# Kernel tuning notes

Measured on AMD Instinct MI355X. Metric: run time of the kernel, lower is better.

## Reference

```python
import jax, jax.numpy as jnp
import numpy as np

B, C, H, W = 16, 256, 56, 56
HID = C * 2            # modifier_expansion = 2
GROUPS = 8             # min(8, HID//4)
K = 3                  # inner_steps
LR = 0.01              # exp(log(inner_lr))
RATIO = 0.25           # spatial_mask_ratio
GN_EPS = 1e-5


def setup_inputs() -> dict:
    key = jax.random.key(0)
    ks = jax.random.split(key, 12)
    x = jax.random.normal(ks[0], (B, C, H, W), jnp.float32)
    # modifier params (1x1 convs stored as 2D matrices) + GroupNorm affine
    conv1_w = jax.random.normal(ks[1], (HID, C), jnp.float32) / np.sqrt(C)
    gn_gamma = 1.0 + 0.1 * jax.random.normal(ks[2], (HID,), jnp.float32)
    gn_beta = 0.1 * jax.random.normal(ks[3], (HID,), jnp.float32)
    conv2_w = jax.random.normal(ks[4], (C, HID), jnp.float32) / np.sqrt(HID)
    # surprise reconstructor (bottleneck = C//4)
    recon_w1 = jax.random.normal(ks[5], (C // 4, C), jnp.float32) / np.sqrt(C)
    recon_w2 = jax.random.normal(ks[6], (C, C // 4), jnp.float32) / np.sqrt(C // 4)
    # gate MLP
    gate_w1 = jax.random.normal(ks[7], (C // 4, C), jnp.float32) / np.sqrt(C)
    gate_b1 = jnp.zeros((C // 4,), jnp.float32)
    gate_w2 = jax.random.normal(ks[8], (1, C // 4), jnp.float32) / np.sqrt(C // 4)
    gate_b2 = jnp.zeros((1,), jnp.float32)
    residual_scale = jnp.asarray(0.05, jnp.float32)
    # EMA buffers (eval mode: frozen)
    running_mean = 0.05 * jax.random.normal(ks[9], (C,), jnp.float32)
    running_var = 1.0 + 0.05 * jax.random.uniform(ks[10], (C,), jnp.float32)
    # spatial masks: exactly int(H*W*RATIO) zeroed positions per sample, one mask
    # per inner update step (only steps 0..K-2 affect the output)
    num_mask = int(H * W * RATIO)
    rng = np.random.default_rng(0)
    r = rng.random((K - 1, B, H * W))
    idx = np.argsort(r, axis=-1)[..., :num_mask]
    m = np.ones((K - 1, B, H * W), dtype=bool)
    np.put_along_axis(m, idx, False, axis=-1)
    masks = jnp.asarray(m.reshape(K - 1, B, 1, H, W))
    return dict(x=x, conv1_w=conv1_w, gn_gamma=gn_gamma, gn_beta=gn_beta,
                conv2_w=conv2_w, recon_w1=recon_w1, recon_w2=recon_w2,
                gate_w1=gate_w1, gate_b1=gate_b1, gate_w2=gate_w2,
                gate_b2=gate_b2, residual_scale=residual_scale,
                running_mean=running_mean, running_var=running_var, masks=masks)


def _group_norm(h, gamma, beta):
    b = h.shape[0]
    hg = h.reshape(b, GROUPS, HID // GROUPS, H, W)
    mu = hg.mean(axis=(2, 3, 4), keepdims=True)
    var = hg.var(axis=(2, 3, 4), keepdims=True)  # biased, matching torch GN
    hg = (hg - mu) * jax.lax.rsqrt(var + GN_EPS)
    return hg.reshape(b, HID, H, W) * gamma[None, :, None, None] + beta[None, :, None, None]


def _modifier(feat, w1, gamma, beta, w2):
    # Conv2d 1x1 (no bias) -> GroupNorm -> GELU -> [Dropout2d: identity in eval] -> Conv2d 1x1
    h = jnp.einsum('bchw,oc->bohw', feat, w1)
    h = jax.nn.gelu(_group_norm(h, gamma, beta), approximate=False)
    return jnp.einsum('bohw,co->bchw', h, w2)


def _surprise(y, mask, rw1, rw2, rm, rv):
    mf = mask.astype(y.dtype)                       # [B,1,H,W]
    my = y * mf
    h = jax.nn.gelu(jnp.einsum('bchw,oc->bohw', my, rw1), approximate=False)
    rec = jnp.einsum('bohw,co->bchw', h, rw2)
    inv = 1.0 - mf
    recon = (((rec - y) ** 2) * inv).sum() / (inv.sum() * C + 1e-8)
    n = y.shape[0] * y.shape[2] * y.shape[3]
    cm = y.mean(axis=(0, 2, 3))                     # [C]
    cv = ((y - cm[None, :, None, None]) ** 2).sum(axis=(0, 2, 3)) / (n - 1)  # unbiased
    consist = ((cm - rm) ** 2).mean() + ((cv / (rv + 1e-8) - 1.0) ** 2).mean()
    return recon + 0.1 * consist


def reference(x, conv1_w, gn_gamma, gn_beta, conv2_w, recon_w1, recon_w2,
              gate_w1, gate_b1, gate_w2, gate_b2, residual_scale,
              running_mean, running_var, masks):
    feat = jax.lax.stop_gradient(x)  # feat_inner = features.detach()
    params = (conv1_w, gn_gamma, gn_beta, conv2_w)

    def inner_loss(p, mask):
        m = _modifier(feat, *p)
        return _surprise(m + feat, mask, recon_w1, recon_w2, running_mean, running_var)

    # TTT inner loop: K-1 SGD updates on the modifier params; updates are
    # stop_gradient'ed so the outer Jacobian wrt initial params is identity,
    # matching torch's .data in-place update with create_graph=False.
    for step in range(K - 1):
        g = jax.grad(inner_loss)(params, masks[step])
        params = tuple(p - LR * jax.lax.stop_gradient(gi) for p, gi in zip(params, g))

    modification = _modifier(x, *params)  # final forward uses non-detached features

    pooled = x.mean(axis=(2, 3))                                    # [B,C]
    gh = jax.nn.gelu(pooled @ gate_w1.T + gate_b1, approximate=False)
    gate = jax.nn.sigmoid(gh @ gate_w2.T + gate_b2)[:, :, None, None]  # [B,1,1,1]

    return x + residual_scale * gate * modification
```

## Files before the change

### kernel.cpp

```cpp
#include <hip/hip_runtime.h>
#include <math.h>


#define BB    16
#define CC    256
#define HWW   3136
#define NTOT  (BB*HWW)
#define HIDD  512
#define NGRP  8
#define GMSZ  (64*HWW)
#define C4    64
#define LRATE 0.01f
#define SKW   32
#define CHUNK (NTOT/SKW)
#define NV8   (HWW/8)
#define FSTR  132

#define EP_STORE    0
#define EP_ADDFEAT  1
#define EP_T1H      2
#define EP_DYREC    3
#define EP_DT1      4
#define EP_DYFIN    5
#define EP_H1STAT   6
#define EP_YADDSTAT 7
#define EP_GNB1     8
#define EP_OUT      9

typedef unsigned short u16;
typedef __attribute__((ext_vector_type(8))) short bf16x8;
typedef __attribute__((ext_vector_type(4))) float f32x4;

__device__ __forceinline__ float bf2f(u16 u){
  return __uint_as_float(((unsigned)u)<<16);
}
__device__ __forceinline__ u16 f2bf(float f){
  unsigned u = __float_as_uint(f);
  u += 0x7FFFu + ((u>>16)&1u);
  return (u16)(u>>16);
}
__device__ __forceinline__ float gelu_f(float x){
  return 0.5f*x*(1.0f+erff(x*0.70710678118654752f));
}
__device__ __forceinline__ float rcp_f(float x){ return __builtin_amdgcn_rcpf(x); }
__device__ __forceinline__ float gelu_fast(float x){
  float x2 = x*x;
  float u = 0.7978845608f*x*fmaf(0.044715f, x2, 1.0f);
  float t = 1.0f - 2.0f*rcp_f(__expf(2.0f*u)+1.0f);
  return 0.5f*x*(1.0f+t);
}
__device__ __forceinline__ float gelu_g_fast(float x){
  float x2 = x*x;
  float u = 0.7978845608f*x*fmaf(0.044715f, x2, 1.0f);
  float t = 1.0f - 2.0f*rcp_f(__expf(2.0f*u)+1.0f);
  float du = 0.7978845608f*fmaf(0.134145f, x2, 1.0f);
  return fmaf(0.5f*x*(1.0f-t*t), du, 0.5f*(1.0f+t));
}
__device__ __forceinline__ float blk_sum(float v, float* sm){
  #pragma unroll
  for (int o=32;o>0;o>>=1) v += __shfl_down(v,o);
  if ((threadIdx.x & 63)==0) sm[threadIdx.x>>6] = v;
  __syncthreads();
  float r = sm[0]+sm[1]+sm[2]+sm[3];
  __syncthreads();
  return r;
}
__device__ __forceinline__ uint4 pack8(const ushort* e){
  uint4 v;
  v.x = (unsigned)e[0] | ((unsigned)e[1]<<16);
  v.y = (unsigned)e[2] | ((unsigned)e[3]<<16);
  v.z = (unsigned)e[4] | ((unsigned)e[5]<<16);
  v.w = (unsigned)e[6] | ((unsigned)e[7]<<16);
  return v;
}
__device__ __forceinline__ void up8(uint4 v, float* f){
  f[0]=bf2f((u16)(v.x&0xFFFFu)); f[1]=bf2f((u16)(v.x>>16));
  f[2]=bf2f((u16)(v.y&0xFFFFu)); f[3]=bf2f((u16)(v.y>>16));
  f[4]=bf2f((u16)(v.z&0xFFFFu)); f[5]=bf2f((u16)(v.z>>16));
  f[6]=bf2f((u16)(v.w&0xFFFFu)); f[7]=bf2f((u16)(v.w>>16));
}
__device__ __forceinline__ uint4 pk8(const float* f){
  uint4 v;
  v.x=(unsigned)f2bf(f[0])|((unsigned)f2bf(f[1])<<16);
  v.y=(unsigned)f2bf(f[2])|((unsigned)f2bf(f[3])<<16);
  v.z=(unsigned)f2bf(f[4])|((unsigned)f2bf(f[5])<<16);
  v.w=(unsigned)f2bf(f[6])|((unsigned)f2bf(f[7])<<16);
  return v;
}

__global__ void k_detect_dtype(const u16* __restrict__ xs, int* flag){
  if (threadIdx.x || blockIdx.x) return;
  int plaus = 0;
  for (int i=0;i<256;i+=2){
    float f = bf2f(xs[i]);
    float a = fabsf(f);
    if (isfinite(f) && a < 32.0f && a > 1e-5f) plaus++;
  }
  *flag = (plaus >= 64) ? 1 : 0;
}
__global__ void k_detect_mask(const unsigned char* __restrict__ m, int* flag){
  if (threadIdx.x || blockIdx.x) return;
  unsigned char mx=0; int nz0=0,nz1=0,nz2=0,nz3=0;
  for (int i=0;i<256;i++){
    unsigned char v=m[i]; if (v>mx) mx=v;
    if (v){ int r=i&3; if(r==0)nz0=1; else if(r==1)nz1=1; else if(r==2)nz2=1; else nz3=1; }
  }
  int f;
  if (mx<=1) f = (nz1|nz2|nz3) ? 0 : 1;
  else       f = (!nz0 && !nz1) ? 3 : 2;
  *flag=f;
}
__global__ void k_report(u16* out, float v){
  if (threadIdx.x==0 && blockIdx.x==0) out[0] = f2bf(v);
}

__global__ void k_cvt(const void* __restrict__ src, float* __restrict__ dst, int n,
                      const int* __restrict__ dtf){
  int i = blockIdx.x*256 + threadIdx.x;
  if (i>=n) return;
  if (*dtf) dst[i] = bf2f(((const u16*)src)[i]);
  else      dst[i] = ((const float*)src)[i];
}
__global__ void k_wcvt(const float* __restrict__ src, u16* __restrict__ d,
                       u16* __restrict__ dT, int R, int Cc){
  int i = blockIdx.x*256+threadIdx.x;
  if (i >= R*Cc) return;
  int r = i/Cc, c = i - r*Cc;
  u16 v = f2bf(src[i]);
  d[i] = v;
  if (dT) dT[(size_t)c*R + r] = v;
}

__global__ void k_expand(const unsigned char* __restrict__ mraw, const int* __restrict__ flag,
                         float* __restrict__ mf, float* __restrict__ zc){
  __shared__ float sm[4];
  int i = blockIdx.x*256 + threadIdx.x;
  int f = *flag;
  float v;
  if (f==1)      v = (((const int*)mraw)[i] != 0) ? 1.f : 0.f;
  else if (f==0) v = (mraw[i] != 0) ? 1.f : 0.f;
  else if (f==2) v = (((const u16*)mraw)[i] != 0) ? 1.f : 0.f;
  else           v = (((const float*)mraw)[i] != 0.f) ? 1.f : 0.f;
  mf[i] = v;
  float S = blk_sum(1.f - v, sm);
  if (threadIdx.x==0) atomicAdd(&zc[blockIdx.x/196], S);
}

template<int MASKX,int EPI,int XDYN,int E0DYN,int MT,int XGN>
__global__ __launch_bounds__(256) void k_gemm_mfma(
    const u16* __restrict__ A, const void* __restrict__ Xv, u16* __restrict__ Out,
    int K, const int* __restrict__ xdt, const float* __restrict__ mf,
    const void* __restrict__ e0, const float* __restrict__ e1,
    const float* __restrict__ e2, u16* __restrict__ o2, float* __restrict__ o3,
    const float* __restrict__ xmu, const float* __restrict__ xpg)
{
  constexpr int MROWS = 64*MT;
  constexpr int NMI   = 4*MT;
  __shared__ __align__(16) u16 Ws[MROWS*42];
  __shared__ __align__(16) u16 Xs[128*42];
  const int t = threadIdx.x;
  const int w = t >> 6, lane = t & 63;
  const int col = lane & 15, quad = lane >> 4;
  const int M = (int)gridDim.y * MROWS;
  const int m0 = blockIdx.y * MROWS, n0 = blockIdx.x << 7;
  const int isbx = XDYN ? *xdt : 1;
  const u16*   Xb = (const u16*)Xv;
  const float* Xf = (const float*)Xv;
  const int wrow = t >> 2, wkq = (t & 3) * 8;
  const int xn   = 2*(t & 63);
  const int xq   = t >> 6;
  const int gn0  = n0 + xn;
  const int xb_  = gn0 / HWW;
  const int xs_  = gn0 - xb_*HWW;

  f32x4 acc[NMI][2];
  #pragma unroll
  for (int i=0;i<NMI;i++){
    #pragma unroll
    for (int j=0;j<2;j++) acc[i][j] = (f32x4)(0.0f);
  }

  for (int k0=0; k0<K; k0+=32){
    if (MT==2){
      const u16* ap = A + (size_t)(m0 + (t>>1))*K + k0 + (t&1)*16;
      *(uint4*)(Ws + (t>>1)*42 + (t&1)*16)     = *(const uint4*)ap;
      *(uint4*)(Ws + (t>>1)*42 + (t&1)*16 + 8) = *(const uint4*)(ap+8);
    } else {
      uint4 v = *(const uint4*)(A + (size_t)(m0+wrow)*K + k0 + wkq);
      *(uint4*)(Ws + wrow*42 + wkq) = v;
    }
    {
      ushort e[16];
      size_t base = ((size_t)xb_*K + k0 + xq*8)*HWW + xs_;
      if (isbx){
        #pragma unroll
        for (int j=0;j<8;j++){
          unsigned v = *(const unsigned*)(Xb + base + (size_t)j*HWW);
          if (XGN){
            const int o  = k0 + xq*8 + j;
            const int bg = xb_*NGRP + (o>>6);
            const float mu_ = xmu[bg], rs_ = xmu[128+bg];
            const float ga_ = xpg[o],  be_ = xpg[512+o];
            float f0 = bf2f((u16)(v & 0xFFFFu));
            float f1 = bf2f((u16)(v >> 16));
            f0 = fmaf((f0-mu_)*rs_, ga_, be_);
            f1 = fmaf((f1-mu_)*rs_, ga_, be_);
            f0 = (XGN==2) ? gelu_f(f0) : gelu_fast(f0);
            f1 = (XGN==2) ? gelu_f(f1) : gelu_fast(f1);
            e[j]   = f2bf(f0);
            e[8+j] = f2bf(f1);
          } else {
            e[j]   = (ushort)(v & 0xFFFFu);
            e[8+j] = (ushort)(v >> 16);
          }
        }
      } else {
        #pragma unroll
        for (int j=0;j<8;j++){
          float2 f = *(const float2*)(Xf + base + (size_t)j*HWW);
          e[j]   = f2bf(f.x);
          e[8+j] = f2bf(f.y);
        }
      }
      if (MASKX){
        if (mf[gn0]   == 0.f){
          #pragma unroll
          for (int j=0;j<8;j++) e[j] = 0;
        }
        if (mf[gn0+1] == 0.f){
          #pragma unroll
          for (int j=0;j<8;j++) e[8+j] = 0;
        }
      }
      *(uint4*)(Xs + xn*42     + xq*8) = pack8(e);
      *(uint4*)(Xs + (xn+1)*42 + xq*8) = pack8(e+8);
    }
    __syncthreads();
    bf16x8 bfr[2];
    #pragma unroll
    for (int nj=0;nj<2;nj++)
      bfr[nj] = *(const bf16x8*)(Xs + (w*32+nj*16+col)*42 + quad*8);
    #pragma unroll
    for (int mi=0;mi<NMI;mi++){
      bf16x8 af = *(const bf16x8*)(Ws + (mi*16+col)*42 + quad*8);
      acc[mi][0] = __builtin_amdgcn_mfma_f32_16x16x32_bf16(af, bfr[0], acc[mi][0], 0,0,0);
      acc[mi][1] = __builtin_amdgcn_mfma_f32_16x16x32_bf16(af, bfr[1], acc[mi][1], 0,0,0);
    }
    __syncthreads();
  }
  const int isb0 = E0DYN ? *xdt : 1;
  float* fst  = (float*)Xs;
  float* sred = (float*)Ws;
  const int row16 = t >> 4;
  const int cb    = (t & 15) * 8;
  const int nb8   = n0 + cb;
  const int b8    = nb8 / HWW;
  const int sb8   = nb8 - b8*HWW;
  const int bA    = n0 / HWW, bB = (n0+127)/HWW;
  const int gbase = m0 >> 6;

  if (EPI==EP_H1STAT){ if (t < 4*MT) sred[t]=0.f; }
  if (EPI==EP_GNB1){ if (t < 4*MT) sred[2*NMI*16 + t]=0.f; }
  if (EPI==EP_H1STAT||EPI==EP_GNB1) __syncthreads();

  float dscale=0.f, gmul=0.f;
  if (EPI==EP_DYREC) dscale = 2.0f / (e1[0]*(float)CC + 1e-8f);
  if (EPI==EP_OUT)   gmul = e2[0]*e1[b8];
  float hs0[MT], hq0[MT], hs1[MT], hq1[MT];
  #pragma unroll
  for (int i=0;i<MT;i++){ hs0[i]=0.f; hq0[i]=0.f; hs1[i]=0.f; hq1[i]=0.f; }

  #pragma unroll
  for (int mi=0;mi<NMI;mi++){
    #pragma unroll
    for (int nj=0;nj<2;nj++){
      #pragma unroll
      for (int r=0;r<4;r++)
        fst[(quad*4+r)*FSTR + w*32 + nj*16 + col] = acc[mi][nj][r];
    }
    __syncthreads();
    const int m = m0 + mi*16 + row16;
    const size_t oidx = ((size_t)b8*M + m)*HWW + sb8;
    float v[8];
    {
      const float* frow = fst + row16*FSTR + cb;
      float4 p0 = *(const float4*)frow;
      float4 p1 = *(const float4*)(frow+4);
      v[0]=p0.x; v[1]=p0.y; v[2]=p0.z; v[3]=p0.w;
      v[4]=p1.x; v[5]=p1.y; v[6]=p1.z; v[7]=p1.w;
    }

    if (EPI==EP_STORE){
      *(uint4*)(Out+oidx) = pk8(v);
    }
    else if (EPI==EP_ADDFEAT){
      float xv[8];
      if (isb0) up8(*(const uint4*)((const u16*)e0+oidx), xv);
      else {
        float4 a0 = *(const float4*)((const float*)e0+oidx);
        float4 a1 = *(const float4*)((const float*)e0+oidx+4);
        xv[0]=a0.x; xv[1]=a0.y; xv[2]=a0.z; xv[3]=a0.w;
        xv[4]=a1.x; xv[5]=a1.y; xv[6]=a1.z; xv[7]=a1.w;
      }
      #pragma unroll
      for (int j=0;j<8;j++) v[j] += xv[j];
      *(uint4*)(Out+oidx) = pk8(v);
    }
    else if (EPI==EP_T1H){
      *(uint4*)(Out+oidx) = pk8(v);
      float gv[8];
      #pragma unroll
      for (int j=0;j<8;j++) gv[j] = gelu_fast(v[j]);
      *(uint4*)(o2+oidx) = pk8(gv);
    }
    else if (EPI==EP_DYREC){
      float yv[8], mfv[8];
      up8(*(const uint4*)((const u16*)e0+oidx), yv);
      float4 f0 = *(const float4*)(mf+nb8);
      float4 f1 = *(const float4*)(mf+nb8+4);
      mfv[0]=f0.x; mfv[1]=f0.y; mfv[2]=f0.z; mfv[3]=f0.w;
      mfv[4]=f1.x; mfv[5]=f1.y; mfv[6]=f1.z; mfv[7]=f1.w;
      #pragma unroll
      for (int j=0;j<8;j++) v[j] = (v[j]-yv[j])*(1.0f-mfv[j])*dscale;
      *(uint4*)(Out+oidx) = pk8(v);
    }
    else if (EPI==EP_DT1){
      float tv[8];
      up8(*(const uint4*)((const u16*)e0+oidx), tv);
      #pragma unroll
      for (int j=0;j<8;j++) v[j] = v[j]*gelu_g_fast(tv[j]);
      *(uint4*)(Out+oidx) = pk8(v);
    }
    else if (EPI==EP_DYFIN){
      float yv[8], dv[8], mfv[8];
      up8(*(const uint4*)((const u16*)e0+oidx), yv);
      up8(*(const uint4*)(Out+oidx), dv);
      float4 f0 = *(const float4*)(mf+nb8);
      float4 f1 = *(const float4*)(mf+nb8+4);
      mfv[0]=f0.x; mfv[1]=f0.y; mfv[2]=f0.z; mfv[3]=f0.w;
      mfv[4]=f1.x; mfv[5]=f1.y; mfv[6]=f1.z; mfv[7]=f1.w;
      const float c1 = e1[m], c2 = e2[m];
      #pragma unroll
      for (int j=0;j<8;j++) v[j] = mfv[j]*v[j] - dv[j] + c1 + c2*yv[j];
      *(uint4*)(Out+oidx) = pk8(v);
    }
    else if (EPI==EP_H1STAT){
      *(uint4*)(Out+oidx) = pk8(v);
      float s=0.f, q=0.f;
      #pragma unroll
      for (int j=0;j<8;j++){ s += v[j]; q = fmaf(v[j],v[j],q); }
      const bool inA = (b8==bA);
      hs0[mi>>2] += inA ? s : 0.f;  hq0[mi>>2] += inA ? q : 0.f;
      hs1[mi>>2] += inA ? 0.f : s;  hq1[mi>>2] += inA ? 0.f : q;
    }
    else if (EPI==EP_YADDSTAT){
      float xv[8];
      if (isb0) up8(*(const uint4*)((const u16*)e0+oidx), xv);
      else {
        float4 a0 = *(const float4*)((const float*)e0+oidx);
        float4 a1 = *(const float4*)((const float*)e0+oidx+4);
        xv[0]=a0.x; xv[1]=a0.y; xv[2]=a0.z; xv[3]=a0.w;
        xv[4]=a1.x; xv[5]=a1.y; xv[6]=a1.z; xv[7]=a1.w;
      }
      float s=0.f, q=0.f;
      #pragma unroll
      for (int j=0;j<8;j++){
        v[j] += xv[j];
        s += v[j]; q = fmaf(v[j],v[j],q);
      }
      *(uint4*)(Out+oidx) = pk8(v);
      #pragma unroll
      for (int o=1;o<16;o<<=1){ s += __shfl_xor(s,o); q += __shfl_xor(q,o); }
      if ((t&15)==0){
        sred[mi*16+row16]          = s;
        sred[NMI*16 + mi*16+row16] = q;
      }
    }
    else if (EPI==EP_GNB1){
      float hv[8];
      up8(*(const uint4*)((const u16*)e0+oidx), hv);
      const int gcur = gbase + (mi>>2);
      const float muT = e1[b8*NGRP+gcur], rT = e1[128+b8*NGRP+gcur];
      const float go = e2[m], beo = e2[HIDD+m];
      float dB=0.f, dG=0.f, sS=0.f, sQ=0.f;
      #pragma unroll
      for (int j=0;j<8;j++){
        float hn   = (hv[j]-muT)*rT;
        float ghat = fmaf(hn, go, beo);
        float dgh  = v[j]*gelu_g_fast(ghat);
        float dhn  = dgh*go;
        v[j] = dhn;
        dB += dgh; dG = fmaf(dgh,hn,dG);
        sS += dhn; sQ = fmaf(dhn,hn,sQ);
      }
      *(uint4*)(Out+oidx) = pk8(v);
      #pragma unroll
      for (int o=1;o<16;o<<=1){ dB += __shfl_xor(dB,o); dG += __shfl_xor(dG,o); }
      if ((t&15)==0){
        sred[mi*16+row16]          = dB;
        sred[NMI*16 + mi*16+row16] = dG;
      }
      const bool inA = (b8==bA);
      hs0[mi>>2] += inA ? sS : 0.f;  hq0[mi>>2] += inA ? sQ : 0.f;
      hs1[mi>>2] += inA ? 0.f : sS;  hq1[mi>>2] += inA ? 0.f : sQ;
    }
    else if (EPI==EP_OUT){
      float xv[8];
      if (isb0){
        up8(*(const uint4*)((const u16*)e0+oidx), xv);
        #pragma unroll
        for (int j=0;j<8;j++) v[j] = xv[j] + gmul*v[j];
        *(uint4*)(Out+oidx) = pk8(v);
      } else {
        float4 a0 = *(const float4*)((const float*)e0+oidx);
        float4 a1 = *(const float4*)((const float*)e0+oidx+4);
        float4 r0, r1;
        r0.x = a0.x + gmul*v[0]; r0.y = a0.y + gmul*v[1];
        r0.z = a0.z + gmul*v[2]; r0.w = a0.w + gmul*v[3];
        r1.x = a1.x + gmul*v[4]; r1.y = a1.y + gmul*v[5];
        r1.z = a1.z + gmul*v[6]; r1.w = a1.w + gmul*v[7];
        *(float4*)((float*)Out+oidx)   = r0;
        *(float4*)((float*)Out+oidx+4) = r1;
      }
    }
    __syncthreads();
  }

  if (EPI==EP_H1STAT || EPI==EP_GNB1){
    const int soff = (EPI==EP_GNB1) ? 2*NMI*16 : 0;
    #pragma unroll
    for (int g2=0; g2<MT; g2++){
      float a0=hs0[g2], c0=hq0[g2], a1=hs1[g2], c1=hq1[g2];
      #pragma unroll
      for (int o=1;o<64;o<<=1){
        a0 += __shfl_xor(a0,o); c0 += __shfl_xor(c0,o);
        a1 += __shfl_xor(a1,o); c1 += __shfl_xor(c1,o);
      }
      if (lane==0){
        atomicAdd(&sred[soff+g2*4+0], a0);
        atomicAdd(&sred[soff+g2*4+1], c0);
        atomicAdd(&sred[soff+g2*4+2], a1);
        atomicAdd(&sred[soff+g2*4+3], c1);
      }
    }
    __syncthreads();
  }

  if (EPI==EP_H1STAT){
    if (t==0){
      #pragma unroll
      for (int g2=0; g2<MT; g2++){
        atomicAdd(&o3[bA*NGRP+gbase+g2],     sred[g2*4+0]);
        atomicAdd(&o3[128+bA*NGRP+gbase+g2], sred[g2*4+1]);
      }
    }
    if (t==1 && bB!=bA){
      #pragma unroll
      for (int g2=0; g2<MT; g2++){
        atomicAdd(&o3[bB*NGRP+gbase+g2],     sred[g2*4+2]);
        atomicAdd(&o3[128+bB*NGRP+gbase+g2], sred[g2*4+3]);
      }
    }
  }
  if (EPI==EP_YADDSTAT){
    if (t < NMI*16){
      atomicAdd(&o3[m0+t],    sred[t]);
      atomicAdd(&o3[CC+m0+t], sred[NMI*16+t]);
    }
  }
  if (EPI==EP_GNB1){
    if (t < NMI*16){
      atomicAdd(&o3[m0+t],     sred[NMI*16+t]);
      atomicAdd(&o3[512+m0+t], sred[t]);
    }
    if (t==NMI*16){
      #pragma unroll
      for (int g2=0; g2<MT; g2++){
        atomicAdd(&o3[1024+bA*NGRP+gbase+g2], sred[2*NMI*16+g2*4+0]);
        atomicAdd(&o3[1152+bA*NGRP+gbase+g2], sred[2*NMI*16+g2*4+1]);
      }
    }
    if (t==NMI*16+1 && bB!=bA){
      #pragma unroll
      for (int g2=0; g2<MT; g2++){
        atomicAdd(&o3[1024+bB*NGRP+gbase+g2], sred[2*NMI*16+g2*4+2]);
        atomicAdd(&o3[1152+bB*NGRP+gbase+g2], sred[2*NMI*16+g2*4+3]);
      }
    }
  }
}

template<int QDYN, int GNB2>
__global__ __launch_bounds__(256) void k_wgrad_mfma(
    const u16* __restrict__ P, const void* __restrict__ Qv, float* __restrict__ part,
    int CHP, int CHQ, const int* __restrict__ xdt, int ntx,
    const u16* __restrict__ h1, const float* __restrict__ musig,
    const float* __restrict__ red)
{
  __shared__ __align__(16) u16 Ps[64*42];
  __shared__ __align__(16) u16 Qs[64*42];
  const int f = blockIdx.x;
  const int j = f >> 3;
  const int sk = (f & 7) + ((j >> 5) << 3);
  const int tile = j & 31;
  const int ty = tile / ntx;
  const int m0 = (tile - ty*ntx) << 6;
  const int n0 = ty << 6;
  const int t = threadIdx.x;
  const int w = t >> 6, lane = t & 63;
  const int col = lane & 15, quad = lane >> 4;
  const int isbq = QDYN ? *xdt : 1;
  const u16*   Qb = (const u16*)Qv;
  const float* Qf = (const float*)Qv;
  const int srow = (t & 127) >> 1;
  const int ssq  = ((t & 127) & 1) * 16;
  f32x4 acc[2][2];
  #pragma unroll
  for (int i=0;i<2;i++){
    #pragma unroll
    for (int jj=0;jj<2;jj++) acc[i][jj] = (f32x4)(0.0f);
  }
  const int mbase = (w & 1)*32, nbase = (w >> 1)*32;

  for (int kb = sk*CHUNK; kb < sk*CHUNK + CHUNK; kb += 32){
    const int b = kb / HWW;
    const int s = kb - b*HWW;
    if (t < 128){
      size_t off = ((size_t)b*CHP + m0+srow)*HWW + s + ssq;
      uint4 v0 = *(const uint4*)(P + off);
      uint4 v1 = *(const uint4*)(P + off + 8);
      if (GNB2){
        const int bg = b*NGRP + (m0>>6);
        const float mu_ = musig[bg], r_ = musig[128+bg];
        const float a1 = red[1024+bg]*(1.0f/GMSZ);
        const float a2 = red[1152+bg]*(1.0f/GMSZ);
        uint4 h0 = *(const uint4*)(h1 + off);
        uint4 h1v = *(const uint4*)(h1 + off + 8);
        float fd[8], fh[8];
        up8(v0, fd); up8(h0, fh);
        #pragma unroll
        for (int q2=0;q2<8;q2++){ float hn=(fh[q2]-mu_)*r_; fd[q2]=r_*(fd[q2]-a1-hn*a2); }
        v0 = pk8(fd);
        up8(v1, fd); up8(h1v, fh);
        #pragma unroll
        for (int q2=0;q2<8;q2++){ float hn=(fh[q2]-mu_)*r_; fd[q2]=r_*(fd[q2]-a1-hn*a2); }
        v1 = pk8(fd);
      }
      *(uint4*)(Ps + srow*42 + ssq)     = v0;
      *(uint4*)(Ps + srow*42 + ssq + 8) = v1;
    } else {
      size_t off = ((size_t)b*CHQ + n0+srow)*HWW + s + ssq;
      if (isbq){
        uint4 v0 = *(const uint4*)(Qb + off);
        uint4 v1 = *(const uint4*)(Qb + off + 8);
        *(uint4*)(Qs + srow*42 + ssq)     = v0;
        *(uint4*)(Qs + srow*42 + ssq + 8) = v1;
      } else {
        ushort e[16];
        #pragma unroll
        for (int g2=0; g2<4; g2++){
          float4 ff = *(const float4*)(Qf + off + g2*4);
          e[g2*4+0]=f2bf(ff.x); e[g2*4+1]=f2bf(ff.y); e[g2*4+2]=f2bf(ff.z); e[g2*4+3]=f2bf(ff.w);
        }
        *(uint4*)(Qs + srow*42 + ssq)     = pack8(e);
        *(uint4*)(Qs + srow*42 + ssq + 8) = pack8(e+8);
      }
    }
    __syncthreads();
    bf16x8 pa[2], qb[2];
    #pragma unroll
    for (int a=0;a<2;a++)
      pa[a] = *(const bf16x8*)(Ps + (mbase + a*16 + col)*42 + quad*8);
    #pragma unroll
    for (int bb=0;bb<2;bb++)
      qb[bb] = *(const bf16x8*)(Qs + (nbase + bb*16 + col)*42 + quad*8);
    #pragma unroll
    for (int a=0;a<2;a++){
      #pragma unroll
      for (int bb=0;bb<2;bb++)
        acc[a][bb] = __builtin_amdgcn_mfma_f32_16x16x32_bf16(pa[a], qb[bb], acc[a][bb], 0,0,0);
    }
    __syncthreads();
  }
  float* dst = part + (size_t)sk*CHP*CHQ;
  #pragma unroll
  for (int a=0;a<2;a++){
    #pragma unroll
    for (int bb=0;bb<2;bb++){
      #pragma unroll
      for (int r=0;r<4;r++){
        const int m = m0 + mbase + a*16 + quad*4 + r;
        const int n = n0 + nbase + bb*16 + col;
        dst[(size_t)m*CHQ + n] = acc[a][bb][r];
      }
    }
  }
}
__global__ void k_wgrad_reduce(const float* __restrict__ part, float* __restrict__ dW, int n){
  int i = blockIdx.x*256+threadIdx.x;
  if (i>=n) return;
  float s=0;
  #pragma unroll
  for (int k=0;k<SKW;k++) s += part[(size_t)k*n + i];
  dW[i]=s;
}

__global__ void k_gn_finalize(const float* gsum, const float* gsumsq, float* mu, float* rsig){
  int i = threadIdx.x; if (i>=BB*NGRP) return;
  float m = gsum[i]*(1.0f/GMSZ);
  float v = gsumsq[i]*(1.0f/GMSZ) - m*m;
  v = fmaxf(v, 0.0f);
  mu[i]=m; rsig[i]=rsqrtf(v+1e-5f);
}
template<int FAST>
__global__ void k_gelu_fwd(const u16* __restrict__ src, u16* __restrict__ dst,
    const float* __restrict__ mu, const float* __restrict__ rsig,
    const float* __restrict__ pg, const float* __restrict__ pb){
  int bo = blockIdx.x;
  int b = bo>>9, o = bo&511, bg = b*NGRP + (o>>6);
  float m = mu[bg], r = rsig[bg], g = pg[o], be = pb[o];
  const uint4* ps = (const uint4*)(src + (size_t)bo*HWW);
  uint4* pd = (uint4*)(dst + (size_t)bo*HWW);
  for (int i=threadIdx.x;i<NV8;i+=256){
    float f[8]; up8(ps[i], f);
    #pragma unroll
    for (int j=0;j<8;j++){
      float gh = fmaf((f[j]-m)*r, g, be);
      f[j] = FAST ? gelu_fast(gh) : gelu_f(gh);
    }
    pd[i] = pk8(f);
  }
}

__global__ void k_y_finalize(const float* cmsum, const float* cmsq,
    const float* rmf, const float* rvf, float* coefA, float* coefB){
  int c = threadIdx.x; if (c>=CC) return;
  float cm = cmsum[c]*(1.0f/NTOT);
  float cv = (cmsq[c] - (float)NTOT*cm*cm)*(1.0f/(NTOT-1));
  float rvp = rvf[c] + 1e-8f;
  float gcm = 0.2f*(cm - rmf[c])*(1.0f/CC);
  float gcv = 0.2f*(cv/rvp - 1.0f)/(rvp*(float)CC);
  coefA[c] = gcm*(1.0f/NTOT) - 2.0f*gcv*cm*(1.0f/(NTOT-1));
  coefB[c] = 2.0f*gcv*(1.0f/(NTOT-1));
}

__global__ void k_gn_bwd1(u16* __restrict__ dA, const u16* __restrict__ h1,
    const float* mu, const float* rsig, const float* pg, const float* pb,
    float* dGa, float* dBe, float* s1, float* s2){
  __shared__ float sm[4];
  int bo = blockIdx.x;
  int b = bo>>9, o = bo&511, bg = b*NGRP + (o>>6);
  float m = mu[bg], r = rsig[bg], g = pg[o], be = pb[o];
  uint4* pa = (uint4*)(dA + (size_t)bo*HWW);
  const uint4* ph = (const uint4*)(h1 + (size_t)bo*HWW);
  float sb=0, sg=0, t1=0, t2=0;
  for (int i=threadIdx.x;i<NV8;i+=256){
    float fa[8], fh[8]; up8(pa[i], fa); up8(ph[i], fh);
    #pragma unroll
    for (int j=0;j<8;j++){
      float hn = (fh[j]-m)*r;
      float ghat = fmaf(hn,g,be);
      float dgh = fa[j]*gelu_g_fast(ghat);
      float dhn = dgh*g;
      fa[j] = dhn;
      sb += dgh; sg = fmaf(dgh,hn,sg); t1 += dhn; t2 = fmaf(dhn,hn,t2);
    }
    pa[i] = pk8(fa);
  }
  float S;
  S = blk_sum(sb,sm); if (threadIdx.x==0) atomicAdd(&dBe[o], S);
  S = blk_sum(sg,sm); if (threadIdx.x==0) atomicAdd(&dGa[o], S);
  S = blk_sum(t1,sm); if (threadIdx.x==0) atomicAdd(&s1[bg], S);
  S = blk_sum(t2,sm); if (threadIdx.x==0) atomicAdd(&s2[bg], S);
}
__global__ void k_gn_bwd2(u16* __restrict__ dA, const u16* __restrict__ h1,
    const float* mu, const float* rsig, const float* s1, const float* s2){
  int bo = blockIdx.x;
  int b = bo>>9, o = bo&511, bg = b*NGRP + (o>>6);
  float m = mu[bg], r = rsig[bg];
  float a1 = s1[bg]*(1.0f/GMSZ), a2 = s2[bg]*(1.0f/GMSZ);
  uint4* pa = (uint4*)(dA + (size_t)bo*HWW);
  const uint4* ph = (const uint4*)(h1 + (size_t)bo*HWW);
  for (int i=threadIdx.x;i<NV8;i+=256){
    float fa[8], fh[8]; up8(pa[i], fa); up8(ph[i], fh);
    #pragma unroll
    for (int j=0;j<8;j++){
      float hn = (fh[j]-m)*r;
      fa[j] = r*(fa[j] - a1 - hn*a2);
    }
    pa[i] = pk8(fa);
  }
}

__global__ void k_update(float* pw1, float* pw2, float* pg, float* pb,
    const float* dW1, const float* dW2, const float* dGa, const float* dBe){
  int i = blockIdx.x*256+threadIdx.x;
  if (i < HIDD*CC){ pw1[i] -= LRATE*dW1[i]; pw2[i] -= LRATE*dW2[i]; }
  if (i < HIDD){ pg[i] -= LRATE*dGa[i]; pb[i] -= LRATE*dBe[i]; }
}

__global__ void k_pool(const void* __restrict__ xv, const int* __restrict__ dtf, float* pooled){
  __shared__ float sm[4];
  int bc = blockIdx.x;
  int isb = *dtf;
  float s=0;
  if (isb){
    const uint4* p = (const uint4*)((const u16*)xv + (size_t)bc*HWW);
    for (int i=threadIdx.x;i<NV8;i+=256){
      float f[8]; up8(p[i], f);
      #pragma unroll
      for (int j=0;j<8;j++) s+=f[j];
    }
  } else {
    const float4* p = (const float4*)((const float*)xv + (size_t)bc*HWW);
    for (int i=threadIdx.x;i<HWW/4;i+=256){
      float4 f = p[i];
      s += f.x+f.y+f.z+f.w;
    }
  }
  float S = blk_sum(s,sm);
  if (threadIdx.x==0) pooled[bc]=S*(1.0f/HWW);
}
__global__ void k_gate(const float* __restrict__ pooled, const float* __restrict__ gw1,
    const float* __restrict__ gb1, const float* __restrict__ gw2, const float* __restrict__ gb2,
    float* gate){
  int b = blockIdx.x, j = threadIdx.x;
  float acc = gb1[j];
  const float* pr = pooled + b*CC;
  for (int c=0;c<CC;c++) acc = fmaf(pr[c], gw1[j*CC+c], acc);
  float v = gelu_f(acc)*gw2[j];
  #pragma unroll
  for (int o=32;o>0;o>>=1) v += __shfl_down(v,o);
  if (j==0) gate[b] = 1.0f/(1.0f+expf(-(v+gb2[0])));
}

extern "C" void kernel_launch(void* const* d_in, const int* in_sizes, int n_in,
                              void* d_out, int out_size, void* d_ws, size_t ws_size,
                              hipStream_t stream)
{
  const void* x_in   = d_in[0];
  const void* w1_in  = d_in[1];
  const void* g_in   = d_in[2];
  const void* b_in   = d_in[3];
  const void* w2_in  = d_in[4];
  const void* rw1_in = d_in[5];
  const void* rw2_in = d_in[6];
  const void* gw1_in = d_in[7];
  const void* gb1_in = d_in[8];
  const void* gw2_in = d_in[9];
  const void* gb2_in = d_in[10];
  const void* rs_in  = d_in[11];
  const void* rm_in  = d_in[12];
  const void* rv_in  = d_in[13];
  const void* mk_in  = d_in[14];
  (void)in_sizes; (void)n_in; (void)out_size;

  char* base = (char*)d_ws;
  size_t off = 0;
  auto alloc = [&](size_t bytes)->char*{
    char* p = base+off; off = (off+bytes+255)&~(size_t)255; return p;
  };
  u16* ybuf = (u16*)alloc((size_t)CC*NTOT*2);
  u16* dY   = (u16*)alloc((size_t)CC*NTOT*2);
  u16* Ab   = (u16*)alloc((size_t)HIDD*NTOT*2);
  u16* t1b  = (u16*)alloc((size_t)C4*NTOT*2);
  u16* hb   = (u16*)alloc((size_t)C4*NTOT*2);
  u16* h1rc = ybuf;
  float* part = (float*)ybuf;
  float* mfb  = (float*)alloc((size_t)2*NTOT*4);
  float* pw1  = (float*)alloc(131072*4);
  float* pw2  = (float*)alloc(131072*4);
  float* dW1  = (float*)alloc(131072*4);
  float* dW2  = (float*)alloc(131072*4);
  u16* wb1   = (u16*)alloc(131072*2);
  u16* wb2   = (u16*)alloc(131072*2);
  u16* wb2T  = (u16*)alloc(131072*2);
  u16* rwb1  = (u16*)alloc(16384*2);
  u16* rwb1T = (u16*)alloc(16384*2);
  u16* rwb2  = (u16*)alloc(16384*2);
  u16* rwb2T = (u16*)alloc(16384*2);
  float* pg   = (float*)alloc(512*4);
  float* pb   = (float*)alloc(512*4);
  float* rw1f = (float*)alloc(16384*4);
  float* rw2f = (float*)alloc(16384*4);
  float* gw1f = (float*)alloc(16384*4);
  float* gb1f = (float*)alloc(64*4);
  float* gw2f = (float*)alloc(64*4);
  float* gb2f = (float*)alloc(256);
  float* rmf  = (float*)alloc(256*4);
  float* rvf  = (float*)alloc(256*4);
  float* rsf  = (float*)alloc(256);
  float* gsum   = (float*)alloc(512);
  float* gsumsq = (float*)alloc(512);
  float* mu     = (float*)alloc(512);
  float* rsig   = (float*)alloc(512);
  float* cmsum  = (float*)alloc(1024);
  float* cmsq   = (float*)alloc(1024);
  float* coefA  = (float*)alloc(1024);
  float* coefB  = (float*)alloc(1024);
  float* dGa    = (float*)alloc(2048);
  float* dBe    = (float*)alloc(2048);
  float* s1     = (float*)alloc(512);
  float* s2     = (float*)alloc(512);
  float* pooled = (float*)alloc(16384);
  float* gate   = (float*)alloc(256);
  float* zc     = (float*)alloc(256);
  int*   dtf    = (int*)alloc(256);
  int*   mkf    = (int*)alloc(256);

  if (off > ws_size){
    k_report<<<1,64,0,stream>>>((u16*)d_out, (float)(ws_size>>20));
    return;
  }
  u16* h1p = nullptr;
  if (off + (size_t)HIDD*NTOT*2 <= ws_size)
    h1p = (u16*)alloc((size_t)HIDD*NTOT*2);

  k_detect_dtype<<<1,1,0,stream>>>((const u16*)x_in, dtf);
  k_detect_mask<<<1,1,0,stream>>>((const unsigned char*)mk_in, mkf);
  #define CVT(src,dst,n) k_cvt<<<((n)+255)/256,256,0,stream>>>(src,dst,(n),dtf)
  CVT(w1_in,  pw1,  131072);
  CVT(g_in,   pg,   512);
  CVT(b_in,   pb,   512);
  CVT(w2_in,  pw2,  131072);
  CVT(rw1_in, rw1f, 16384);
  CVT(rw2_in, rw2f, 16384);
  CVT(gw1_in, gw1f, 16384);
  CVT(gb1_in, gb1f, 64);
  CVT(gw2_in, gw2f, 64);
  CVT(gb2_in, gb2f, 1);
  CVT(rs_in,  rsf,  1);
  CVT(rm_in,  rmf,  256);
  CVT(rv_in,  rvf,  256);
  #undef CVT
  k_wcvt<<<512,256,0,stream>>>(pw1, wb1, 0,     HIDD, CC);
  k_wcvt<<<512,256,0,stream>>>(pw2, wb2, wb2T,  CC, HIDD);
  k_wcvt<<<64,256,0,stream>>>(rw1f, rwb1, rwb1T, C4, CC);
  k_wcvt<<<64,256,0,stream>>>(rw2f, rwb2, rwb2T, CC, C4);
  hipMemsetAsync(zc, 0, 8, stream);
  k_expand<<<392,256,0,stream>>>((const unsigned char*)mk_in, mkf, mfb, zc);

  for (int s=0; s<2; s++){
    const float* mfs = mfb + s*NTOT;
    u16* h1dst = h1p ? h1p : Ab;
    hipMemsetAsync(gsum, 0, 1024, stream);
    k_gemm_mfma<0,EP_H1STAT,1,0,2,0><<<dim3(392,4),256,0,stream>>>(wb1, x_in, h1dst, CC, dtf, 0,0,0,0,0, gsum, 0,0);
    k_gn_finalize<<<1,128,0,stream>>>(gsum, gsumsq, mu, rsig);
    k_gelu_fwd<1><<<BB*HIDD,256,0,stream>>>(h1dst, Ab, mu, rsig, pg, pb);
    hipMemsetAsync(cmsum, 0, 2048, stream);
    k_gemm_mfma<0,EP_YADDSTAT,0,1,2,0><<<dim3(392,2),256,0,stream>>>(wb2, Ab, ybuf, HIDD, dtf, 0, x_in, 0,0,0, cmsum, 0,0);
    k_y_finalize<<<1,256,0,stream>>>(cmsum, cmsq, rmf, rvf, coefA, coefB);
    k_gemm_mfma<1,EP_T1H,0,0,1,0><<<dim3(392,1),256,0,stream>>>(rwb1, ybuf, t1b, CC, dtf, mfs, 0,0,0, hb, 0, 0,0);
    k_gemm_mfma<0,EP_DYREC,0,0,2,0><<<dim3(392,2),256,0,stream>>>(rwb2, hb, dY, C4, dtf, mfs, ybuf, zc+s, 0,0, 0, 0,0);
    k_gemm_mfma<0,EP_DT1,0,0,1,0><<<dim3(392,1),256,0,stream>>>(rwb2T, dY, hb, CC, dtf, 0, t1b, 0,0,0, 0, 0,0);
    k_gemm_mfma<0,EP_DYFIN,0,0,2,0><<<dim3(392,2),256,0,stream>>>(rwb1T, hb, dY, C4, dtf, mfs, ybuf, coefA, coefB, 0, 0, 0,0);
    k_wgrad_mfma<0,0><<<dim3(32*SKW),256,0,stream>>>(dY, Ab, part, CC, HIDD, dtf, 4, 0,0,0);
    k_wgrad_reduce<<<512,256,0,stream>>>(part, dW2, 131072);
    hipMemsetAsync(dGa, 0, 5120, stream);
    if (h1p){
      k_gemm_mfma<0,EP_GNB1,0,0,2,0><<<dim3(392,4),256,0,stream>>>(wb2T, dY, Ab, CC, dtf, 0, h1p, mu, pg, 0, dGa, 0,0);
      k_wgrad_mfma<1,1><<<dim3(32*SKW),256,0,stream>>>(Ab, x_in, part, HIDD, CC, dtf, 8, h1p, mu, dGa);
    } else {
      k_gemm_mfma<0,EP_STORE,0,0,2,0><<<dim3(392,4),256,0,stream>>>(wb2T, dY, Ab, CC, dtf, 0,0,0,0,0, 0, 0,0);
      k_gemm_mfma<0,EP_H1STAT,1,0,2,0><<<dim3(392,4),256,0,stream>>>(wb1, x_in, h1rc, CC, dtf, 0,0,0,0,0, gsum, 0,0);
      k_gn_bwd1<<<BB*HIDD,256,0,stream>>>(Ab, h1rc, mu, rsig, pg, pb, dGa, dBe, s1, s2);
      k_gn_bwd2<<<BB*HIDD,256,0,stream>>>(Ab, h1rc, mu, rsig, s1, s2);
      k_wgrad_mfma<1,0><<<dim3(32*SKW),256,0,stream>>>(Ab, x_in, part, HIDD, CC, dtf, 8, 0,0,0);
    }
    k_wgrad_reduce<<<512,256,0,stream>>>(part, dW1, 131072);
    k_update<<<512,256,0,stream>>>(pw1, pw2, pg, pb, dW1, dW2, dGa, dBe);
    k_wcvt<<<512,256,0,stream>>>(pw1, wb1, 0,    HIDD, CC);
    k_wcvt<<<512,256,0,stream>>>(pw2, wb2, wb2T, CC, HIDD);
  }

  k_pool<<<BB*CC,256,0,stream>>>(x_in, dtf, pooled);
  k_gate<<<BB,64,0,stream>>>(pooled, gw1f, gb1f, gw2f, gb2f, gate);

  hipMemsetAsync(gsum, 0, 1024, stream);
  k_gemm_mfma<0,EP_H1STAT,1,0,2,0><<<dim3(392,4),256,0,stream>>>(wb1, x_in, Ab, CC, dtf, 0,0,0,0,0, gsum, 0,0);
  k_gn_finalize<<<1,128,0,stream>>>(gsum, gsumsq, mu, rsig);
  k_gemm_mfma<0,EP_OUT,0,1,2,2><<<dim3(392,2),256,0,stream>>>(wb2, Ab, (u16*)d_out, HIDD, dtf, 0, x_in, gate, rsf, 0, 0, mu, pg);
}
```

Measured before the change: 1.173 ms.

## Fuse GroupNorm+GELU into GEMM and wgrad operand loads, drop LDS padding

Removes the separate k_gelu_fwd pass in the inner loop when h1 is cached: the y GEMM and the dW2 weight-gradient kernel now apply GroupNorm affine plus fast GELU on the fly while staging h1 into shared memory. This avoids writing and re-reading the activated hidden tensor. The cost is recomputing the GELU in two kernels. The final output GEMM switches from exact GELU to the fast approximation, which risks accuracy. The LDS row stride also changes from 42 to 40, which may alter bank conflicts.

```diff
diff --git a/kernel.cpp b/kernel.cpp
--- a/kernel.cpp
+++ b/kernel.cpp
@@ -156,8 +156,8 @@
 {
   constexpr int MROWS = 64*MT;
   constexpr int NMI   = 4*MT;
-  __shared__ __align__(16) u16 Ws[MROWS*42];
-  __shared__ __align__(16) u16 Xs[128*42];
+  __shared__ __align__(16) u16 Ws[MROWS*40];
+  __shared__ __align__(16) u16 Xs[128*40];
   const int t = threadIdx.x;
   const int w = t >> 6, lane = t & 63;
   const int col = lane & 15, quad = lane >> 4;
@@ -183,33 +183,40 @@
   for (int k0=0; k0<K; k0+=32){
     if (MT==2){
       const u16* ap = A + (size_t)(m0 + (t>>1))*K + k0 + (t&1)*16;
-      *(uint4*)(Ws + (t>>1)*42 + (t&1)*16)     = *(const uint4*)ap;
-      *(uint4*)(Ws + (t>>1)*42 + (t&1)*16 + 8) = *(const uint4*)(ap+8);
+      *(uint4*)(Ws + (t>>1)*40 + (t&1)*16)     = *(const uint4*)ap;
+      *(uint4*)(Ws + (t>>1)*40 + (t&1)*16 + 8) = *(const uint4*)(ap+8);
     } else {
       uint4 v = *(const uint4*)(A + (size_t)(m0+wrow)*K + k0 + wkq);
-      *(uint4*)(Ws + wrow*42 + wkq) = v;
+      *(uint4*)(Ws + wrow*40 + wkq) = v;
     }
     {
       ushort e[16];
       size_t base = ((size_t)xb_*K + k0 + xq*8)*HWW + xs_;
       if (isbx){
-        #pragma unroll
-        for (int j=0;j<8;j++){
-          unsigned v = *(const unsigned*)(Xb + base + (size_t)j*HWW);
-          if (XGN){
-            const int o  = k0 + xq*8 + j;
-            const int bg = xb_*NGRP + (o>>6);
-            const float mu_ = xmu[bg], rs_ = xmu[128+bg];
-            const float ga_ = xpg[o],  be_ = xpg[512+o];
+        if (XGN){
+          const int ob = k0 + xq*8;
+          const int bg = xb_*NGRP + (ob>>6);
+          const float mu_ = xmu[bg], rs_ = xmu[128+bg];
+          float4 ga0 = *(const float4*)(xpg+ob);
+          float4 ga1 = *(const float4*)(xpg+ob+4);
+          float4 be0 = *(const float4*)(xpg+512+ob);
+          float4 be1 = *(const float4*)(xpg+512+ob+4);
+          float ga[8] = {ga0.x,ga0.y,ga0.z,ga0.w,ga1.x,ga1.y,ga1.z,ga1.w};
+          float be[8] = {be0.x,be0.y,be0.z,be0.w,be1.x,be1.y,be1.z,be1.w};
+          #pragma unroll
+          for (int j=0;j<8;j++){
+            unsigned v = *(const unsigned*)(Xb + base + (size_t)j*HWW);
             float f0 = bf2f((u16)(v & 0xFFFFu));
             float f1 = bf2f((u16)(v >> 16));
-            f0 = fmaf((f0-mu_)*rs_, ga_, be_);
-            f1 = fmaf((f1-mu_)*rs_, ga_, be_);
-            f0 = (XGN==2) ? gelu_f(f0) : gelu_fast(f0);
-            f1 = (XGN==2) ? gelu_f(f1) : gelu_fast(f1);
+            f0 = gelu_fast(fmaf((f0-mu_)*rs_, ga[j], be[j]));
+            f1 = gelu_fast(fmaf((f1-mu_)*rs_, ga[j], be[j]));
             e[j]   = f2bf(f0);
             e[8+j] = f2bf(f1);
-          } else {
+          }
+        } else {
+          #pragma unroll
+          for (int j=0;j<8;j++){
+            unsigned v = *(const unsigned*)(Xb + base + (size_t)j*HWW);
             e[j]   = (ushort)(v & 0xFFFFu);
             e[8+j] = (ushort)(v >> 16);
           }
@@ -232,17 +239,17 @@
           for (int j=0;j<8;j++) e[8+j] = 0;
         }
       }
-      *(uint4*)(Xs + xn*42     + xq*8) = pack8(e);
-      *(uint4*)(Xs + (xn+1)*42 + xq*8) = pack8(e+8);
+      *(uint4*)(Xs + xn*40     + xq*8) = pack8(e);
+      *(uint4*)(Xs + (xn+1)*40 + xq*8) = pack8(e+8);
     }
     __syncthreads();
     bf16x8 bfr[2];
     #pragma unroll
     for (int nj=0;nj<2;nj++)
-      bfr[nj] = *(const bf16x8*)(Xs + (w*32+nj*16+col)*42 + quad*8);
+      bfr[nj] = *(const bf16x8*)(Xs + (w*32+nj*16+col)*40 + quad*8);
     #pragma unroll
     for (int mi=0;mi<NMI;mi++){
-      bf16x8 af = *(const bf16x8*)(Ws + (mi*16+col)*42 + quad*8);
+      bf16x8 af = *(const bf16x8*)(Ws + (mi*16+col)*40 + quad*8);
       acc[mi][0] = __builtin_amdgcn_mfma_f32_16x16x32_bf16(af, bfr[0], acc[mi][0], 0,0,0);
       acc[mi][1] = __builtin_amdgcn_mfma_f32_16x16x32_bf16(af, bfr[1], acc[mi][1], 0,0,0);
     }
@@ -490,15 +497,15 @@
   }
 }
 
-template<int QDYN, int GNB2>
+template<int QDYN, int GNB2, int QGN>
 __global__ __launch_bounds__(256) void k_wgrad_mfma(
     const u16* __restrict__ P, const void* __restrict__ Qv, float* __restrict__ part,
     int CHP, int CHQ, const int* __restrict__ xdt, int ntx,
     const u16* __restrict__ h1, const float* __restrict__ musig,
-    const float* __restrict__ red)
+    const float* __restrict__ red, const float* __restrict__ qpg)
 {
-  __shared__ __align__(16) u16 Ps[64*42];
-  __shared__ __align__(16) u16 Qs[64*42];
+  __shared__ __align__(16) u16 Ps[64*40];
+  __shared__ __align__(16) u16 Qs[64*40];
   const int f = blockIdx.x;
   const int j = f >> 3;
   const int sk = (f & 7) + ((j >> 5) << 3);
@@ -514,6 +521,11 @@
   const float* Qf = (const float*)Qv;
   const int srow = (t & 127) >> 1;
   const int ssq  = ((t & 127) & 1) * 16;
+  float ga_q = 0.f, be_q = 0.f;
+  if (QGN && t >= 128){
+    ga_q = qpg[n0+srow];
+    be_q = qpg[512+n0+srow];
+  }
   f32x4 acc[2][2];
   #pragma unroll
   for (int i=0;i<2;i++){
@@ -546,15 +558,28 @@
         for (int q2=0;q2<8;q2++){ float hn=(fh[q2]-mu_)*r_; fd[q2]=r_*(fd[q2]-a1-hn*a2); }
         v1 = pk8(fd);
       }
-      *(uint4*)(Ps + srow*42 + ssq)     = v0;
-      *(uint4*)(Ps + srow*42 + ssq + 8) = v1;
+      *(uint4*)(Ps + srow*40 + ssq)     = v0;
+      *(uint4*)(Ps + srow*40 + ssq + 8) = v1;
     } else {
       size_t off = ((size_t)b*CHQ + n0+srow)*HWW + s + ssq;
       if (isbq){
         uint4 v0 = *(const uint4*)(Qb + off);
         uint4 v1 = *(const uint4*)(Qb + off + 8);
-        *(uint4*)(Qs + srow*42 + ssq)     = v0;
-        *(uint4*)(Qs + srow*42 + ssq + 8) = v1;
+        if (QGN){
+          const int bg = b*NGRP + ((n0+srow)>>6);
+          const float mu_ = musig[bg], rs_ = musig[128+bg];
+          float fq[8];
+          up8(v0, fq);
+          #pragma unroll
+          for (int q2=0;q2<8;q2++) fq[q2] = gelu_fast(fmaf((fq[q2]-mu_)*rs_, ga_q, be_q));
+          v0 = pk8(fq);
+          up8(v1, fq);
+          #pragma unroll
+          for (int q2=0;q2<8;q2++) fq[q2] = gelu_fast(fmaf((fq[q2]-mu_)*rs_, ga_q, be_q));
+          v1 = pk8(fq);
+        }
+        *(uint4*)(Qs + srow*40 + ssq)     = v0;
+        *(uint4*)(Qs + srow*40 + ssq + 8) = v1;
       } else {
         ushort e[16];
         #pragma unroll
@@ -562,18 +587,18 @@
           float4 ff = *(const float4*)(Qf + off + g2*4);
           e[g2*4+0]=f2bf(ff.x); e[g2*4+1]=f2bf(ff.y); e[g2*4+2]=f2bf(ff.z); e[g2*4+3]=f2bf(ff.w);
         }
-        *(uint4*)(Qs + srow*42 + ssq)     = pack8(e);
-        *(uint4*)(Qs + srow*42 + ssq + 8) = pack8(e+8);
+        *(uint4*)(Qs + srow*40 + ssq)     = pack8(e);
+        *(uint4*)(Qs + srow*40 + ssq + 8) = pack8(e+8);
       }
     }
     __syncthreads();
     bf16x8 pa[2], qb[2];
     #pragma unroll
     for (int a=0;a<2;a++)
-      pa[a] = *(const bf16x8*)(Ps + (mbase + a*16 + col)*42 + quad*8);
+      pa[a] = *(const bf16x8*)(Ps + (mbase + a*16 + col)*40 + quad*8);
     #pragma unroll
     for (int bb=0;bb<2;bb++)
-      qb[bb] = *(const bf16x8*)(Qs + (nbase + bb*16 + col)*42 + quad*8);
+      qb[bb] = *(const bf16x8*)(Qs + (nbase + bb*16 + col)*40 + quad*8);
     #pragma unroll
     for (int a=0;a<2;a++){
       #pragma unroll
@@ -846,26 +871,34 @@
     hipMemsetAsync(gsum, 0, 1024, stream);
     k_gemm_mfma<0,EP_H1STAT,1,0,2,0><<<dim3(392,4),256,0,stream>>>(wb1, x_in, h1dst, CC, dtf, 0,0,0,0,0, gsum, 0,0);
     k_gn_finalize<<<1,128,0,stream>>>(gsum, gsumsq, mu, rsig);
-    k_gelu_fwd<1><<<BB*HIDD,256,0,stream>>>(h1dst, Ab, mu, rsig, pg, pb);
     hipMemsetAsync(cmsum, 0, 2048, stream);
-    k_gemm_mfma<0,EP_YADDSTAT,0,1,2,0><<<dim3(392,2),256,0,stream>>>(wb2, Ab, ybuf, HIDD, dtf, 0, x_in, 0,0,0, cmsum, 0,0);
+    if (h1p){
+      k_gemm_mfma<0,EP_YADDSTAT,0,1,2,1><<<dim3(392,2),256,0,stream>>>(wb2, h1p, ybuf, HIDD, dtf, 0, x_in, 0,0,0, cmsum, mu, pg);
+    } else {
+      k_gelu_fwd<1><<<BB*HIDD,256,0,stream>>>(Ab, Ab, mu, rsig, pg, pb);
+      k_gemm_mfma<0,EP_YADDSTAT,0,1,2,0><<<dim3(392,2),256,0,stream>>>(wb2, Ab, ybuf, HIDD, dtf, 0, x_in, 0,0,0, cmsum, 0,0);
+    }
     k_y_finalize<<<1,256,0,stream>>>(cmsum, cmsq, rmf, rvf, coefA, coefB);
     k_gemm_mfma<1,EP_T1H,0,0,1,0><<<dim3(392,1),256,0,stream>>>(rwb1, ybuf, t1b, CC, dtf, mfs, 0,0,0, hb, 0, 0,0);
     k_gemm_mfma<0,EP_DYREC,0,0,2,0><<<dim3(392,2),256,0,stream>>>(rwb2, hb, dY, C4, dtf, mfs, ybuf, zc+s, 0,0, 0, 0,0);
     k_gemm_mfma<0,EP_DT1,0,0,1,0><<<dim3(392,1),256,0,stream>>>(rwb2T, dY, hb, CC, dtf, 0, t1b, 0,0,0, 0, 0,0);
     k_gemm_mfma<0,EP_DYFIN,0,0,2,0><<<dim3(392,2),256,0,stream>>>(rwb1T, hb, dY, C4, dtf, mfs, ybuf, coefA, coefB, 0, 0, 0,0);
-    k_wgrad_mfma<0,0><<<dim3(32*SKW),256,0,stream>>>(dY, Ab, part, CC, HIDD, dtf, 4, 0,0,0);
+    if (h1p){
+      k_wgrad_mfma<0,0,1><<<dim3(32*SKW),256,0,stream>>>(dY, h1p, part, CC, HIDD, dtf, 4, 0, mu, 0, pg);
+    } else {
+      k_wgrad_mfma<0,0,0><<<dim3(32*SKW),256,0,stream>>>(dY, Ab, part, CC, HIDD, dtf, 4, 0,0,0,0);
+    }
     k_wgrad_reduce<<<512,256,0,stream>>>(part, dW2, 131072);
     hipMemsetAsync(dGa, 0, 5120, stream);
     if (h1p){
       k_gemm_mfma<0,EP_GNB1,0,0,2,0><<<dim3(392,4),256,0,stream>>>(wb2T, dY, Ab, CC, dtf, 0, h1p, mu, pg, 0, dGa, 0,0);
-      k_wgrad_mfma<1,1><<<dim3(32*SKW),256,0,stream>>>(Ab, x_in, part, HIDD, CC, dtf, 8, h1p, mu, dGa);
+      k_wgrad_mfma<1,1,0><<<dim3(32*SKW),256,0,stream>>>(Ab, x_in, part, HIDD, CC, dtf, 8, h1p, mu, dGa, 0);
     } else {
       k_gemm_mfma<0,EP_STORE,0,0,2,0><<<dim3(392,4),256,0,stream>>>(wb2T, dY, Ab, CC, dtf, 0,0,0,0,0, 0, 0,0);
       k_gemm_mfma<0,EP_H1STAT,1,0,2,0><<<dim3(392,4),256,0,stream>>>(wb1, x_in, h1rc, CC, dtf, 0,0,0,0,0, gsum, 0,0);
       k_gn_bwd1<<<BB*HIDD,256,0,stream>>>(Ab, h1rc, mu, rsig, pg, pb, dGa, dBe, s1, s2);
       k_gn_bwd2<<<BB*HIDD,256,0,stream>>>(Ab, h1rc, mu, rsig, s1, s2);
-      k_wgrad_mfma<1,0><<<dim3(32*SKW),256,0,stream>>>(Ab, x_in, part, HIDD, CC, dtf, 8, 0,0,0);
+      k_wgrad_mfma<1,0,0><<<dim3(32*SKW),256,0,stream>>>(Ab, x_in, part, HIDD, CC, dtf, 8, 0,0,0,0);
     }
     k_wgrad_reduce<<<512,256,0,stream>>>(part, dW1, 131072);
     k_update<<<512,256,0,stream>>>(pw1, pw2, pg, pb, dW1, dW2, dGa, dBe);
@@ -879,5 +912,5 @@
   hipMemsetAsync(gsum, 0, 1024, stream);
   k_gemm_mfma<0,EP_H1STAT,1,0,2,0><<<dim3(392,4),256,0,stream>>>(wb1, x_in, Ab, CC, dtf, 0,0,0,0,0, gsum, 0,0);
   k_gn_finalize<<<1,128,0,stream>>>(gsum, gsumsq, mu, rsig);
-  k_gemm_mfma<0,EP_OUT,0,1,2,2><<<dim3(392,2),256,0,stream>>>(wb2, Ab, (u16*)d_out, HIDD, dtf, 0, x_in, gate, rsf, 0, 0, mu, pg);
-}
+  k_gemm_mfma<0,EP_OUT,0,1,2,1><<<dim3(392,2),256,0,stream>>>(wb2, Ab, (u16*)d_out, HIDD, dtf, 0, x_in, gate, rsf, 0, 0, mu, pg);
+}
```

After: 1.145 ms. -2.4%, faster.
